# Kernel optimization log

Measured on AMD Instinct MI355X. Metric: run time of the kernel, lower is better.

The kernel has to match this reference:

```python
import jax, jax.numpy as jnp
import numpy as np

N = 50000
E = 800000
D = 3            # stalk dimension d
H = 64           # hidden_channels
OUT_SHAPE = (3, 3)


def setup_inputs() -> dict:
    key = jax.random.key(0)
    k1, k2, k3 = jax.random.split(key, 3)
    x = jax.random.normal(k1, (N, D * H), dtype=jnp.float32)
    # torch.nn.Linear(2*H, prod(out_shape), bias=False): weight [out, in]
    W = jax.random.normal(k2, (int(np.prod(OUT_SHAPE)), 2 * H), dtype=jnp.float32) * 0.08
    edge_index = jax.random.randint(k3, (2, E), 0, N, dtype=jnp.int64)
    return {"x": x, "W": W, "edge_index": edge_index}


def reference(x, W, edge_index):
    row, col = edge_index[0], edge_index[1]
    x_row = x[row]                       # [E, D*H] gather
    x_col = x[col]                       # [E, D*H] gather
    x_cat = jnp.concatenate([x_row, x_col], axis=-1)       # [E, 2*D*H]
    x_cat = x_cat.reshape(-1, D, 2 * H).sum(axis=1)         # [E, 2*H] sum-pool over d
    maps = jnp.tanh(x_cat @ W.T)                            # [E, 9]
    return maps.reshape(-1, OUT_SHAPE[0], OUT_SHAPE[1])     # [E, 3, 3]
```

## Files before the change

### kernel.cpp

```cpp
#include <hip/hip_runtime.h>
#include <cstddef>


typedef float v4f __attribute__((ext_vector_type(4)));

__device__ __forceinline__ float tanh_fast(float s) {
    float ex = __builtin_amdgcn_exp2f(s * 2.88539008f);
    return fmaf(-2.0f, __builtin_amdgcn_rcpf(ex + 1.0f), 1.0f);
}

__global__ __launch_bounds__(256) void node_proj_kernel(
    const float* __restrict__ x, const float* __restrict__ W,
    _Float16* __restrict__ A, _Float16* __restrict__ B, int nnodes)
{
    __shared__ float ws[9 * 64];
    __shared__ float wd[9 * 64];
    for (int k = threadIdx.x; k < 9 * 64; k += 256) {
        int j = k >> 6, c = k & 63;
        float w0 = W[j * 128 + c], w1 = W[j * 128 + 64 + c];
        ws[k] = 0.5f * (w0 + w1);
        wd[k] = 0.5f * (w0 - w1);
    }
    __syncthreads();

    const int quad = threadIdx.x >> 2;
    const int q    = threadIdx.x & 3;
    const int n    = blockIdx.x * 64 + quad;
    if (n >= nnodes) return;

    const float* xr = x + (size_t)n * 192;

    float ps[9], pd[9];
#pragma unroll
    for (int j = 0; j < 9; ++j) { ps[j] = 0.0f; pd[j] = 0.0f; }

#pragma unroll
    for (int ii = 0; ii < 4; ++ii) {
        const int c = 16 * ii + 4 * q;
        v4f x0 = *(const v4f*)(xr + c);
        v4f x1 = *(const v4f*)(xr + 64 + c);
        v4f x2 = *(const v4f*)(xr + 128 + c);
        v4f u = x0 + x2;
        v4f su = u + x1;
        v4f du = u - x1;
#pragma unroll
        for (int j = 0; j < 9; ++j) {
            v4f a = *(const v4f*)(ws + j * 64 + c);
            v4f b = *(const v4f*)(wd + j * 64 + c);
            ps[j] = fmaf(a.x, su.x, ps[j]); ps[j] = fmaf(a.y, su.y, ps[j]);
            ps[j] = fmaf(a.z, su.z, ps[j]); ps[j] = fmaf(a.w, su.w, ps[j]);
            pd[j] = fmaf(b.x, du.x, pd[j]); pd[j] = fmaf(b.y, du.y, pd[j]);
            pd[j] = fmaf(b.z, du.z, pd[j]); pd[j] = fmaf(b.w, du.w, pd[j]);
        }
    }

#pragma unroll
    for (int j = 0; j < 9; ++j) {
        ps[j] += __shfl_xor(ps[j], 1); ps[j] += __shfl_xor(ps[j], 2);
        pd[j] += __shfl_xor(pd[j], 1); pd[j] += __shfl_xor(pd[j], 2);
    }

    _Float16* Ar = A + (size_t)n * 9;
    _Float16* Br = B + (size_t)n * 9;
    for (int j = q; j < 9; j += 4) {
        Ar[j] = (_Float16)(ps[j] + pd[j]);
        Br[j] = (_Float16)(ps[j] - pd[j]);
    }
}

__global__ __launch_bounds__(256) void edge_map_kernel(
    const int* __restrict__ ei, const _Float16* __restrict__ A,
    const _Float16* __restrict__ B, float* __restrict__ out,
    int nedges, int total)
{
    int t = blockIdx.x * 256 + threadIdx.x;
    if (t >= total) return;
    int e = (int)(((long long)t * 954437177LL) >> 33);
    int j = t - e * 9;
    int row = ei[e];
    int col = ei[nedges + e];
    float s = (float)A[row * 9 + j] + (float)B[col * 9 + j];
    out[t] = tanh_fast(s);
}

extern "C" void kernel_launch(void* const* d_in, const int* in_sizes, int n_in,
                              void* d_out, int out_size, void* d_ws, size_t ws_size,
                              hipStream_t stream) {
    const float* x  = (const float*)d_in[0];
    const float* W  = (const float*)d_in[1];
    const int*   ei = (const int*)d_in[2];
    float* out = (float*)d_out;

    const int nnodes = in_sizes[0] / 192;
    const int nedges = in_sizes[2] / 2;

    _Float16* A = (_Float16*)d_ws;
    _Float16* B = A + (size_t)nnodes * 9;

    const int blocks1 = (nnodes + 63) / 64;
    node_proj_kernel<<<blocks1, 256, 0, stream>>>(x, W, A, B, nnodes);

    const int total   = nedges * 9;
    const int blocks2 = (total + 255) / 256;
    edge_map_kernel<<<blocks2, 256, 0, stream>>>(ei, A, B, out, nedges, total);
}
```

Before: 34.48 us.

## Pad node tables to 16 halves and process one edge per thread via LDS staging

Node projection tables A and B are padded from 9 to 16 fp16 entries per node so each edge can fetch its row with one 16-byte vector load plus one scalar. The edge kernel now assigns one edge per thread instead of one output element per thread. It computes all 9 tanh values, stages them in shared memory, and writes them back as coalesced stores. This cuts the index loads and the divide-by-9 math per output, but adds an LDS round trip and a barrier, uses more workspace, and launches 9x fewer threads.

Result: faster. 32.25 us (-6.5%).

```diff
diff --git a/kernel.cpp b/kernel.cpp
--- a/kernel.cpp
+++ b/kernel.cpp
@@ -3,6 +3,7 @@
 
 
 typedef float v4f __attribute__((ext_vector_type(4)));
+typedef _Float16 v8h __attribute__((ext_vector_type(8)));
 
 __device__ __forceinline__ float tanh_fast(float s) {
     float ex = __builtin_amdgcn_exp2f(s * 2.88539008f);
@@ -60,8 +61,8 @@
         pd[j] += __shfl_xor(pd[j], 1); pd[j] += __shfl_xor(pd[j], 2);
     }
 
-    _Float16* Ar = A + (size_t)n * 9;
-    _Float16* Br = B + (size_t)n * 9;
+    _Float16* Ar = A + (size_t)n * 16;
+    _Float16* Br = B + (size_t)n * 16;
     for (int j = q; j < 9; j += 4) {
         Ar[j] = (_Float16)(ps[j] + pd[j]);
         Br[j] = (_Float16)(ps[j] - pd[j]);
@@ -70,17 +71,32 @@
 
 __global__ __launch_bounds__(256) void edge_map_kernel(
     const int* __restrict__ ei, const _Float16* __restrict__ A,
-    const _Float16* __restrict__ B, float* __restrict__ out,
-    int nedges, int total)
+    const _Float16* __restrict__ B, float* __restrict__ out, int nedges)
 {
-    int t = blockIdx.x * 256 + threadIdx.x;
-    if (t >= total) return;
-    int e = (int)(((long long)t * 954437177LL) >> 33);
-    int j = t - e * 9;
-    int row = ei[e];
-    int col = ei[nedges + e];
-    float s = (float)A[row * 9 + j] + (float)B[col * 9 + j];
-    out[t] = tanh_fast(s);
+    __shared__ float so[256 * 9];
+    const int e0 = blockIdx.x * 256;
+    const int e  = e0 + threadIdx.x;
+    const int cnt = min(256, nedges - e0);
+
+    if (e < nedges) {
+        int row = ei[e];
+        int col = ei[nedges + e];
+        const _Float16* Ar = A + (size_t)row * 16;
+        const _Float16* Br = B + (size_t)col * 16;
+        v8h a8 = *(const v8h*)Ar;  _Float16 a8e = Ar[8];
+        v8h b8 = *(const v8h*)Br;  _Float16 b8e = Br[8];
+        float* sl = so + threadIdx.x * 9;
+#pragma unroll
+        for (int j = 0; j < 8; ++j)
+            sl[j] = tanh_fast((float)a8[j] + (float)b8[j]);
+        sl[8] = tanh_fast((float)a8e + (float)b8e);
+    }
+    __syncthreads();
+
+    float* ob = out + (size_t)e0 * 9;
+    const int tot = cnt * 9;
+    for (int k = threadIdx.x; k < tot; k += 256)
+        ob[k] = so[k];
 }
 
 extern "C" void kernel_launch(void* const* d_in, const int* in_sizes, int n_in,
@@ -95,12 +111,11 @@
     const int nedges = in_sizes[2] / 2;
 
     _Float16* A = (_Float16*)d_ws;
-    _Float16* B = A + (size_t)nnodes * 9;
+    _Float16* B = A + (size_t)nnodes * 16;
 
     const int blocks1 = (nnodes + 63) / 64;
     node_proj_kernel<<<blocks1, 256, 0, stream>>>(x, W, A, B, nnodes);
 
-    const int total   = nedges * 9;
-    const int blocks2 = (total + 255) / 256;
-    edge_map_kernel<<<blocks2, 256, 0, stream>>>(ei, A, B, out, nedges, total);
+    const int blocks2 = (nedges + 255) / 256;
+    edge_map_kernel<<<blocks2, 256, 0, stream>>>(ei, A, B, out, nedges);
 }
```
